# Optimization experiments

Hardware: AMD Instinct MI355X
Metric: run time of the kernel (lower is better)

## Reference

```python
import jax, jax.numpy as jnp
import numpy as np

B, T, D = 2, 1024, 1024
H, DK, DV = 16, 64, 128   # head_dim=64, head_v_dim=128 (expand_v=2)
F_HID, CONV = 2816, 4
EPS = 1e-6


def rmsnorm(x, w, eps=EPS):
    return x * jax.lax.rsqrt(jnp.mean(x * x, -1, keepdims=True) + eps) * w


def l2norm(x, eps=1e-6):
    return x * jax.lax.rsqrt(jnp.sum(x * x, -1, keepdims=True) + eps)


def short_conv(x, w):
    # causal depthwise conv1d (kernel CONV, no bias) + silu; x: [B,T,C], w: [C,K]
    K = w.shape[1]
    xp = jnp.pad(x, ((0, 0), (K - 1, 0), (0, 0)))
    y = jax.lax.conv_general_dilated(
        xp, w.T[:, None, :], (1,), 'VALID',
        dimension_numbers=('NWC', 'WIO', 'NWC'), feature_group_count=w.shape[0])
    return jax.nn.silu(y)


def gated_delta_rule(q, k, v, g, beta):
    # q,k: [B,T,H,DK], v: [B,T,H,DV], g,beta: [B,T,H]
    scale = q.shape[-1] ** -0.5
    q = l2norm(q) * scale
    k = l2norm(k)

    def step(S, inp):
        qt, kt, vt, gt, bt = inp          # S: [B,H,DK,DV]
        S = S * jnp.exp(gt)[..., None, None]
        err = jnp.einsum('bhk,bhkv->bhv', kt, S)
        vt = (vt - err) * bt[..., None]
        S = S + kt[..., :, None] * vt[..., None, :]
        ot = jnp.einsum('bhk,bhkv->bhv', qt, S)
        return S, ot

    S0 = jnp.zeros((q.shape[0], H, DK, DV), q.dtype)
    inputs = tuple(jnp.moveaxis(a, 1, 0) for a in (q, k, v, g, beta))
    _, o = jax.lax.scan(step, S0, inputs)
    return jnp.moveaxis(o, 0, 1)  # [B,T,H,DV]


def setup_inputs():
    key = jax.random.key(0)
    ks = jax.random.split(key, 20)
    w = lambda k, shape, s=0.02: jax.random.normal(k, shape, jnp.float32) * s
    return {
        'x': jax.random.normal(ks[0], (B, T, D), jnp.float32),
        'norm1_w': jnp.ones((D,), jnp.float32),
        'norm2_w': jnp.ones((D,), jnp.float32),
        'Wq': w(ks[1], (D, H * DK)),
        'Wk': w(ks[2], (D, H * DK)),
        'Wv': w(ks[3], (D, H * DV)),
        'conv_q': w(ks[4], (H * DK, CONV), 0.3),
        'conv_k': w(ks[5], (H * DK, CONV), 0.3),
        'conv_v': w(ks[6], (H * DV, CONV), 0.3),
        'Wa': w(ks[7], (D, H)),
        'Wb': w(ks[8], (D, H)),
        'dt_bias': jnp.log(jnp.expm1(jax.random.uniform(ks[9], (H,), minval=0.001, maxval=0.1))),
        'A_log': jnp.log(jax.random.uniform(ks[10], (H,), minval=1.0, maxval=16.0)),
        'Wg': w(ks[11], (D, H * DV)),
        'o_norm_w': jnp.ones((DV,), jnp.float32),
        'Wo': w(ks[12], (H * DV, D)),
        'W1': w(ks[13], (D, F_HID)),
        'W3': w(ks[14], (D, F_HID)),
        'W2': w(ks[15], (F_HID, D)),
    }


def reference(x, norm1_w, norm2_w, Wq, Wk, Wv, conv_q, conv_k, conv_v,
              Wa, Wb, dt_bias, A_log, Wg, o_norm_w, Wo, W1, W3, W2):
    # --- pre-norm + GatedDeltaNet ---
    h = rmsnorm(x, norm1_w)
    q = short_conv(h @ Wq, conv_q).reshape(B, T, H, DK)
    k = short_conv(h @ Wk, conv_k).reshape(B, T, H, DK)
    v = short_conv(h @ Wv, conv_v).reshape(B, T, H, DV)
    beta = jax.nn.sigmoid(h @ Wb)                                  # [B,T,H]
    g = -jnp.exp(A_log) * jax.nn.softplus(h @ Wa + dt_bias)       # [B,T,H] decay log
    o = gated_delta_rule(q, k, v, g, beta)                         # [B,T,H,DV]
    gate = (h @ Wg).reshape(B, T, H, DV)
    o = rmsnorm(o, o_norm_w, 1e-5) * jax.nn.silu(gate)             # gated RMSNorm
    x = x + o.reshape(B, T, H * DV) @ Wo                           # residual 1
    # --- pre-norm + SwiGLU FFN ---
    h2 = rmsnorm(x, norm2_w)
    ffn = (jax.nn.silu(h2 @ W1) * (h2 @ W3)) @ W2
    return x + ffn
```

## Files before the change

### kernel.cpp

```cpp
#include <hip/hip_runtime.h>
#include <hip/hip_bf16.h>
#include <math.h>

#define B_  2
#define T_  1024
#define D_  1024
#define H_  16
#define DK_ 64
#define DV_ 128
#define FH_ 2816
#define M_  (B_ * T_)
#define C_  64
#define NCH (T_ / C_)

typedef __attribute__((ext_vector_type(8))) short bf16x8;
typedef __attribute__((ext_vector_type(4))) float f32x4;

__global__ __launch_bounds__(256) void rmsnorm_k(
    const float* __restrict__ x, const float* __restrict__ w,
    float* __restrict__ outf, __hip_bfloat16* __restrict__ outb,
    int D, float eps) {
  const int row = blockIdx.x;
  const float* xr = x + (size_t)row * D;
  float ss = 0.f;
  for (int i = threadIdx.x; i < D; i += blockDim.x) { float v = xr[i]; ss += v * v; }
  for (int off = 32; off > 0; off >>= 1) ss += __shfl_xor(ss, off, 64);
  __shared__ float wsum[4];
  __shared__ float s_scale;
  const int lane = threadIdx.x & 63, wid = threadIdx.x >> 6;
  if (lane == 0) wsum[wid] = ss;
  __syncthreads();
  if (threadIdx.x == 0) {
    float tot = 0.f;
    const int nw = blockDim.x >> 6;
    for (int i = 0; i < nw; ++i) tot += wsum[i];
    s_scale = rsqrtf(tot / (float)D + eps);
  }
  __syncthreads();
  const float sc = s_scale;
  for (int i = threadIdx.x; i < D; i += blockDim.x) {
    const float v = xr[i] * sc * w[i];
    if (outf) outf[(size_t)row * D + i] = v;
    if (outb) outb[(size_t)row * D + i] = __float2bfloat16(v);
  }
}

__global__ __launch_bounds__(256) void transpose_bf16_k(
    const float* __restrict__ W, __hip_bfloat16* __restrict__ Wt, int K, int N) {
  __shared__ float t[32][33];
  const int k0 = blockIdx.y * 32, n0 = blockIdx.x * 32;
  const int c = threadIdx.x & 31, r = threadIdx.x >> 5;
#pragma unroll
  for (int i = 0; i < 4; ++i)
    t[r + 8 * i][c] = W[(size_t)(k0 + r + 8 * i) * N + n0 + c];
  __syncthreads();
#pragma unroll
  for (int i = 0; i < 4; ++i)
    Wt[(size_t)(n0 + r + 8 * i) * K + k0 + c] = __float2bfloat16(t[c][r + 8 * i]);
}

__device__ __forceinline__ void gload_lds16(const void* g, void* l) {
  __builtin_amdgcn_global_load_lds(
      (const __attribute__((address_space(1))) void*)g,
      (__attribute__((address_space(3))) void*)l, 16, 0, 0);
}

template<int BM, int BN>
__global__ __launch_bounds__(256) void mfma_gemm_k(
    const __hip_bfloat16* __restrict__ A, const __hip_bfloat16* __restrict__ Bt,
    const float* __restrict__ res, void* __restrict__ Cout,
    int M, int N, int K, int mode) {
  __shared__ __hip_bfloat16 As[2][BM * 64];
  __shared__ __hip_bfloat16 Bs[2][BN * 64];
  constexpr int MF = BM / 32;
  constexpr int NF = BN / 32;
  const int tid = threadIdx.x;
  const int lane = tid & 63;
  const int wv = tid >> 6;
  const int wm = (wv >> 1) * (BM / 2), wn = (wv & 1) * (BN / 2);
  const int bm = blockIdx.y * BM, bn = blockIdx.x * BN;
  const int l15 = lane & 15, lq8 = (lane >> 4) * 8;
  const int ar = tid >> 2;
  const int ac = (tid & 3) * 8;
  const size_t Abase = (size_t)(bm + ar) * K + ac;
  const size_t Bbase = (size_t)(bn + ar) * K + ac;
  f32x4 acc[MF][NF];
#pragma unroll
  for (int i = 0; i < MF; ++i)
#pragma unroll
    for (int j = 0; j < NF; ++j) acc[i][j] = (f32x4){0.f, 0.f, 0.f, 0.f};

  auto stage = [&](int buf, int k0) {
#pragma unroll
    for (int s = 0; s < 2; ++s) {
      const int kk = k0 + 32 * s;
      char* dA = (char*)&As[buf][s * BM * 32] + tid * 16;
      gload_lds16(A + Abase + kk, dA);
      if constexpr (BM == 128)
        gload_lds16(A + Abase + (size_t)64 * K + kk, dA + 4096);
      char* dB = (char*)&Bs[buf][s * BN * 32] + tid * 16;
      gload_lds16(Bt + Bbase + kk, dB);
      if constexpr (BN == 128)
        gload_lds16(Bt + Bbase + (size_t)64 * K + kk, dB + 4096);
    }
  };

  stage(0, 0);
  __syncthreads();
  int cur = 0;
#pragma unroll 2
  for (int k0 = 0; k0 < K; k0 += 64) {
    if (k0 + 64 < K) stage(cur ^ 1, k0 + 64);
#pragma unroll
    for (int s = 0; s < 2; ++s) {
      bf16x8 af[MF], bfr[NF];
#pragma unroll
      for (int i = 0; i < MF; ++i)
        af[i] = *(const bf16x8*)(&As[cur][s * BM * 32] + (wm + i * 16 + l15) * 32 + lq8);
#pragma unroll
      for (int j = 0; j < NF; ++j)
        bfr[j] = *(const bf16x8*)(&Bs[cur][s * BN * 32] + (wn + j * 16 + l15) * 32 + lq8);
#pragma unroll
      for (int i = 0; i < MF; ++i)
#pragma unroll
        for (int j = 0; j < NF; ++j)
          acc[i][j] = __builtin_amdgcn_mfma_f32_16x16x32_bf16(af[i], bfr[j], acc[i][j], 0, 0, 0);
    }
    __syncthreads();
    cur ^= 1;
  }
  const int r0 = (lane >> 4) * 4;
#pragma unroll
  for (int i = 0; i < MF; ++i) {
#pragma unroll
    for (int j = 0; j < NF; ++j) {
      const int row = bm + wm + i * 16 + r0;
      const int col = bn + wn + j * 16 + l15;
#pragma unroll
      for (int r = 0; r < 4; ++r) {
        const size_t idx = (size_t)(row + r) * N + col;
        const float a = acc[i][j][r];
        if (mode == 0) ((float*)Cout)[idx] = a;
        else if (mode == 1) ((float*)Cout)[idx] = a + res[idx];
        else {
          const float s = res[idx];
          ((__hip_bfloat16*)Cout)[idx] =
              __float2bfloat16(s * (1.f / (1.f + __expf(-s))) * a);
        }
      }
    }
  }
}

__global__ __launch_bounds__(256) void skinny_k(
    const float* __restrict__ h, const float* __restrict__ Wa,
    const float* __restrict__ Wb, float* __restrict__ pa,
    float* __restrict__ pb, int K) {
  __shared__ float hl[D_];
  __shared__ float red[8][32];
  const int row = blockIdx.x;
  const int tid = threadIdx.x;
  {
    const float4* src = (const float4*)(h + (size_t)row * K);
    ((float4*)hl)[tid] = src[tid];
  }
  __syncthreads();
  const int col = tid & 31, sub = tid >> 5;
  const float* W = (col < 16) ? Wa : Wb;
  const int cc = col & 15;
  float s = 0.f;
  const int kk0 = sub * 128;
  for (int k = kk0; k < kk0 + 128; ++k) s += hl[k] * W[k * H_ + cc];
  red[sub][col] = s;
  __syncthreads();
  if (tid < 32) {
    float t = 0.f;
#pragma unroll
    for (int i = 0; i < 8; ++i) t += red[i][tid];
    if (tid < 16) pa[(size_t)row * H_ + tid] = t;
    else          pb[(size_t)row * H_ + tid - 16] = t;
  }
}

__global__ __launch_bounds__(256) void conv_silu_k(
    const float* __restrict__ src, const float* __restrict__ w,
    float* __restrict__ dst, int C, int sstr, int soff) {
  const int bt = blockIdx.x;
  const int b = bt / T_, t = bt % T_;
  const float* s = src + (size_t)b * T_ * sstr + soff;
  for (int c = threadIdx.x; c < C; c += blockDim.x) {
    const float w0 = w[c * 4 + 0], w1 = w[c * 4 + 1],
                w2 = w[c * 4 + 2], w3 = w[c * 4 + 3];
    float acc = s[(size_t)t * sstr + c] * w3;
    if (t >= 1) acc += s[(size_t)(t - 1) * sstr + c] * w2;
    if (t >= 2) acc += s[(size_t)(t - 2) * sstr + c] * w1;
    if (t >= 3) acc += s[(size_t)(t - 3) * sstr + c] * w0;
    dst[(size_t)bt * C + c] = acc * (1.f / (1.f + __expf(-acc)));
  }
}

__global__ void beta_g_k(const float* __restrict__ pa, const float* __restrict__ pb,
                         const float* __restrict__ dtb, const float* __restrict__ Alog,
                         float* __restrict__ g, float* __restrict__ beta, int n) {
  const int i = blockIdx.x * blockDim.x + threadIdx.x;
  if (i >= n) return;
  const int h = i & (H_ - 1);
  const float xx = pa[i] + dtb[h];
  const float sp = (xx > 20.f) ? xx : log1pf(expf(xx));
  g[i] = -expf(Alog[h]) * sp;
  beta[i] = 1.f / (1.f + expf(-pb[i]));
}

__global__ __launch_bounds__(64) void l2norm_k(float* __restrict__ q, float scale) {
  const size_t row = blockIdx.x;
  const int lane = threadIdx.x;
  const float v = q[row * 64 + lane];
  float ss = v * v;
  for (int off = 32; off > 0; off >>= 1) ss += __shfl_xor(ss, off, 64);
  q[row * 64 + lane] = v * rsqrtf(ss + 1e-6f) * scale;
}

__global__ __launch_bounds__(256) void chunk_prep_k(
    const float* __restrict__ q, float* __restrict__ k, float* __restrict__ v,
    const float* __restrict__ g, const float* __restrict__ beta,
    float* __restrict__ qkd, float* __restrict__ kdt, float* __restrict__ gam,
    float* __restrict__ wt) {
  const int task = blockIdx.x;
  const int bh = task >> 4, n = task & (NCH - 1);
  const int b = bh >> 4, h = bh & 15;
  const int t0 = n * C_;
  const int tid = threadIdx.x;
  __shared__ float lk[C_][68];
  __shared__ float Gs[C_][68];
  __shared__ float Xs[C_][100];
  __shared__ float Td[4][16][17];
  __shared__ float lb[C_], lgam[C_], lbeta[C_], lbg[C_];
  {
    const int r = tid >> 2, cq = (tid & 3) * 16;
    const float* src = k + (((size_t)b * T_ + t0 + r) * H_ + h) * DK_ + cq;
#pragma unroll
    for (int i = 0; i < 4; ++i)
      *(float4*)&lk[r][cq + 4 * i] = ((const float4*)src)[i];
  }
  if (tid < 64) {
    const size_t gi = ((size_t)b * T_ + t0 + tid) * H_ + h;
    float xx = g[gi];
    const float bb = beta[gi];
    lbeta[tid] = bb;
#pragma unroll
    for (int off = 1; off < 64; off <<= 1) {
      float y = __shfl_up(xx, off, 64);
      if (tid >= off) xx += y;
    }
    lb[tid] = xx;
    const float gm = __expf(xx);
    lgam[tid] = gm;
    lbg[tid] = bb * gm;
  }
  __syncthreads();
  const int r4g = (tid >> 4) * 4;
  const int sl = tid & 15;
  {
    const float* qg = q + (((size_t)b * T_ + t0) * H_ + h) * DK_;
    float accA[4][4] = {};
    float accQ[4][4] = {};
    for (int d = 0; d < 64; d += 4) {
      float4 kt[4], ks[4], qt[4];
#pragma unroll
      for (int i = 0; i < 4; ++i) kt[i] = *(const float4*)&lk[r4g + i][d];
#pragma unroll
      for (int j = 0; j < 4; ++j) ks[j] = *(const float4*)&lk[sl + 16 * j][d];
#pragma unroll
      for (int i = 0; i < 4; ++i) qt[i] = *(const float4*)(qg + (size_t)(r4g + i) * (H_ * DK_) + d);
#pragma unroll
      for (int i = 0; i < 4; ++i)
#pragma unroll
        for (int j = 0; j < 4; ++j) {
          accA[i][j] += kt[i].x * ks[j].x + kt[i].y * ks[j].y + kt[i].z * ks[j].z + kt[i].w * ks[j].w;
          accQ[i][j] += qt[i].x * ks[j].x + qt[i].y * ks[j].y + qt[i].z * ks[j].z + qt[i].w * ks[j].w;
        }
    }
    float* qo = qkd + (size_t)task * 4096;
#pragma unroll
    for (int i = 0; i < 4; ++i)
#pragma unroll
      for (int j = 0; j < 4; ++j) {
        const int t = r4g + i, s = sl + 16 * j;
        const float dec = (s <= t) ? __expf(lb[t] - lb[s]) : 0.f;
        Gs[t][s] = (t > s) ? lbeta[t] * accA[i][j] * dec : 0.f;
        qo[t * 64 + s] = accQ[i][j] * dec;
      }
  }
  {
    const int s = tid >> 2, dq = (tid & 3) * 16;
    const float e = __expf(lb[63] - lb[s]);
    float* dst = kdt + (size_t)task * 4096 + s * 64 + dq;
#pragma unroll
    for (int m = 0; m < 4; ++m) {
      float4 kv = *(const float4*)&lk[s][dq + 4 * m];
      kv.x *= e; kv.y *= e; kv.z *= e; kv.w *= e;
      *(float4*)(dst + 4 * m) = kv;
    }
  }
  if (tid < 64) gam[(size_t)task * 64 + tid] = lgam[tid];
  __syncthreads();
  if (tid < 64) {
    const int blk = tid >> 4, cI = tid & 15;
    float Xc[16];
#pragma unroll
    for (int t = 0; t < 16; ++t) Xc[t] = (t == cI) ? 1.f : 0.f;
#pragma unroll
    for (int t = 1; t < 16; ++t) {
      float acc = 0.f;
#pragma unroll
      for (int s = 0; s < t; ++s)
        acc += Gs[blk * 16 + t][blk * 16 + s] * Xc[s];
      Xc[t] -= acc;
    }
#pragma unroll
    for (int t = 0; t < 16; ++t) Td[blk][t][cI] = Xc[t];
  } else {
    for (int idx = tid - 64; idx < 64 * 96; idx += 192) {
      const int t = idx / 96, c = idx % 96;
      Xs[t][c] = lbeta[t] * v[(((size_t)b * T_ + t0 + t) * H_ + h) * DV_ + c];
    }
  }
  __syncthreads();
  const int rt = tid & 15;
  const int cg = tid >> 4;
#pragma unroll 1
  for (int half = 0; half < 2; ++half) {
#pragma unroll
    for (int bi = 0; bi < 4; ++bi) {
      if (bi > 0) {
        float acc[6] = {0.f, 0.f, 0.f, 0.f, 0.f, 0.f};
        for (int kk = 0; kk < 16 * bi; ++kk) {
          const float gvv = Gs[16 * bi + rt][kk];
#pragma unroll
          for (int c = 0; c < 6; ++c) acc[c] += gvv * Xs[kk][cg * 6 + c];
        }
#pragma unroll
        for (int c = 0; c < 6; ++c) Xs[16 * bi + rt][cg * 6 + c] -= acc[c];
      }
      float y[6] = {0.f, 0.f, 0.f, 0.f, 0.f, 0.f};
#pragma unroll
      for (int s = 0; s < 16; ++s) {
        const float tv = Td[bi][rt][s];
#pragma unroll
        for (int c = 0; c < 6; ++c) y[c] += tv * Xs[16 * bi + s][cg * 6 + c];
      }
#pragma unroll
      for (int c = 0; c < 6; ++c) Xs[16 * bi + rt][cg * 6 + c] = y[c];
    }
    __syncthreads();
    if (half == 0) {
      for (int idx = tid; idx < 64 * 96; idx += 256) {
        const int t = idx / 96, c = idx % 96;
        v[(((size_t)b * T_ + t0 + t) * H_ + h) * DV_ + c] = Xs[t][c];
      }
      __syncthreads();
      for (int idx = tid; idx < 64 * 96; idx += 256) {
        const int t = idx / 96, c = idx % 96;
        if (c < 32)
          Xs[t][c] = lbeta[t] * v[(((size_t)b * T_ + t0 + t) * H_ + h) * DV_ + 96 + c];
        else
          Xs[t][c] = lbg[t] * lk[t][c - 32];
      }
      __syncthreads();
    } else {
      for (int idx = tid; idx < 64 * 32; idx += 256) {
        const int t = idx >> 5, cc = idx & 31;
        v[(((size_t)b * T_ + t0 + t) * H_ + h) * DV_ + 96 + cc] = Xs[t][cc];
      }
      {
        const int dk = tid & 63, tg = tid >> 6;
        float buf[16];
#pragma unroll
        for (int j = 0; j < 16; ++j) buf[j] = Xs[16 * tg + j][32 + dk];
        float* dst = wt + (size_t)task * 4096 + dk * 64 + 16 * tg;
#pragma unroll
        for (int m = 0; m < 4; ++m)
          *(float4*)(dst + 4 * m) =
              make_float4(buf[4 * m], buf[4 * m + 1], buf[4 * m + 2], buf[4 * m + 3]);
      }
    }
  }
}

__global__ __launch_bounds__(256) void chunk_rec_k(
    const float* __restrict__ WT, float* __restrict__ u,
    const float* __restrict__ kdtT, const float* __restrict__ gam,
    float* __restrict__ Sst) {
  const int bh = blockIdx.x & 31, cg = blockIdx.x >> 5;
  const int b = bh >> 4, h = bh & 15;
  const int c0 = cg * 16;
  const int tid = threadIdx.x;
  const int w = tid >> 6;
  const int lane = tid & 63;
  const int L15 = lane & 15;
  const int t4 = L15 * 4;
  const int c = w * 4 + (lane >> 4);
  const int iot = tid >> 2;
  const int ioq = (tid & 3) * 4;

  __shared__ float Wt[2][64 * 64];
  __shared__ float Kt[2][64 * 64];
  __shared__ float SsT[16][68];
  __shared__ float UbT[16][68];
  __shared__ float Ub0[64][17];

  float Sr[4];
#pragma unroll
  for (int i = 0; i < 4; ++i) Sr[i] = 0.f;
#pragma unroll
  for (int i = 0; i < 4; ++i) SsT[c][t4 + i] = 0.f;

  {
    const float* sW = WT + (size_t)(bh * NCH) * 4096 + w * 1024 + lane * 4;
    const float* sK = kdtT + (size_t)(bh * NCH) * 4096 + w * 1024 + lane * 4;
    char* lW = (char*)&Wt[0][w * 1024] + lane * 16;
    char* lK = (char*)&Kt[0][w * 1024] + lane * 16;
#pragma unroll
    for (int i = 0; i < 4; ++i) {
      gload_lds16(sW + i * 256, lW + i * 1024);
      gload_lds16(sK + i * 256, lK + i * 1024);
    }
  }
  __syncthreads();

#pragma unroll 1
  for (int n = 0; n < NCH; ++n) {
    const int cur = n & 1, nx = cur ^ 1;
    const int task = bh * NCH + n;
    const int t0 = n * C_;
    const int n1 = (n + 1 < NCH) ? n + 1 : NCH - 1;
    const int task1 = bh * NCH + n1;
    const float gC = gam[(size_t)task * 64 + 63];

    const float4 uv = *(const float4*)(
        u + (((size_t)b * T_ + t0 + iot) * H_ + h) * DV_ + c0 + ioq);
    {
      const float* sW = WT + (size_t)task1 * 4096 + w * 1024 + lane * 4;
      const float* sK = kdtT + (size_t)task1 * 4096 + w * 1024 + lane * 4;
      char* lW = (char*)&Wt[nx][w * 1024] + lane * 16;
      char* lK = (char*)&Kt[nx][w * 1024] + lane * 16;
#pragma unroll
      for (int i = 0; i < 4; ++i) {
        gload_lds16(sW + i * 256, lW + i * 1024);
        gload_lds16(sK + i * 256, lK + i * 1024);
      }
    }
    __builtin_amdgcn_sched_barrier(0);
    {
      float4 sv;
      sv.x = SsT[ioq + 0][iot]; sv.y = SsT[ioq + 1][iot];
      sv.z = SsT[ioq + 2][iot]; sv.w = SsT[ioq + 3][iot];
      *(float4*)(Sst + (size_t)task * 8192 + iot * 128 + c0 + ioq) = sv;
    }
    float4 srow[16];
#pragma unroll
    for (int g = 0; g < 16; ++g) srow[g] = *(const float4*)&SsT[c][4 * g];
    float acc[4] = {0.f, 0.f, 0.f, 0.f};
#pragma unroll
    for (int g = 0; g < 16; ++g) {
      const float sj[4] = {srow[g].x, srow[g].y, srow[g].z, srow[g].w};
#pragma unroll
      for (int j = 0; j < 4; ++j) {
        const float4 wv = *(const float4*)&Wt[cur][(4 * g + j) * 64 + t4];
        acc[0] += wv.x * sj[j]; acc[1] += wv.y * sj[j];
        acc[2] += wv.z * sj[j]; acc[3] += wv.w * sj[j];
      }
    }
    Ub0[iot][ioq + 0] = uv.x; Ub0[iot][ioq + 1] = uv.y;
    Ub0[iot][ioq + 2] = uv.z; Ub0[iot][ioq + 3] = uv.w;
    __syncthreads();

#pragma unroll
    for (int i = 0; i < 4; ++i)
      UbT[c][t4 + i] = Ub0[t4 + i][c] - acc[i];
    float4 urow[16];
#pragma unroll
    for (int g = 0; g < 16; ++g) urow[g] = *(const float4*)&UbT[c][4 * g];
    float ac2[4] = {0.f, 0.f, 0.f, 0.f};
#pragma unroll
    for (int g = 0; g < 16; ++g) {
      const float uj[4] = {urow[g].x, urow[g].y, urow[g].z, urow[g].w};
#pragma unroll
      for (int j = 0; j < 4; ++j) {
        const float4 kv = *(const float4*)&Kt[cur][(4 * g + j) * 64 + t4];
        ac2[0] += kv.x * uj[j]; ac2[1] += kv.y * uj[j];
        ac2[2] += kv.z * uj[j]; ac2[3] += kv.w * uj[j];
      }
    }
#pragma unroll
    for (int i = 0; i < 4; ++i) {
      Sr[i] = gC * Sr[i] + ac2[i];
      SsT[c][t4 + i] = Sr[i];
    }
    __syncthreads();

    {
      float4 ov;
      ov.x = UbT[ioq + 0][iot]; ov.y = UbT[ioq + 1][iot];
      ov.z = UbT[ioq + 2][iot]; ov.w = UbT[ioq + 3][iot];
      *(float4*)(u + (((size_t)b * T_ + t0 + iot) * H_ + h) * DV_ + c0 + ioq) = ov;
    }
  }
}

__global__ __launch_bounds__(128) void chunk_o_k(
    const float* __restrict__ q, const float* __restrict__ qkd,
    const float* __restrict__ ub, const float* __restrict__ Sst,
    const float* __restrict__ gam, const float* __restrict__ gate,
    const float* __restrict__ onw, __hip_bfloat16* __restrict__ go) {
  const int task = blockIdx.x;
  const int bh = task >> 4, n = task & 15;
  const int b = bh >> 4, h = bh & 15;
  const int t0 = n * C_;
  const int tid = threadIdx.x;
  const int rowg = tid >> 4, colg = tid & 15;
  const int r8 = rowg * 8, c4 = colg * 4;
  __shared__ float At[64][68];
  __shared__ float Bs[64][132];
  __shared__ float lgam[64];
  if (tid < 64) lgam[tid] = gam[(size_t)task * 64 + tid];
  __syncthreads();
  const int t2 = tid >> 1, dh = (tid & 1) * 32;
  {
    const float* src = q + (((size_t)b * T_ + t0 + t2) * H_ + h) * DK_ + dh;
    const float sc = lgam[t2];
#pragma unroll
    for (int i = 0; i < 8; ++i) {
      const float4 v = ((const float4*)src)[i];
      At[dh + 4 * i + 0][t2] = v.x * sc; At[dh + 4 * i + 1][t2] = v.y * sc;
      At[dh + 4 * i + 2][t2] = v.z * sc; At[dh + 4 * i + 3][t2] = v.w * sc;
    }
  }
  {
    const float* src = Sst + (size_t)task * 8192 + t2 * 128 + (tid & 1) * 64;
    float* dst = &Bs[t2][(tid & 1) * 64];
#pragma unroll
    for (int i = 0; i < 16; ++i) ((float4*)dst)[i] = ((const float4*)src)[i];
  }
  __syncthreads();
  float acc[8][8];
#pragma unroll
  for (int i = 0; i < 8; ++i)
#pragma unroll
    for (int c = 0; c < 8; ++c) acc[i][c] = 0.f;
#pragma unroll 1
  for (int ph = 0; ph < 2; ++ph) {
    for (int kb = 0; kb < 64; kb += 4) {
#pragma unroll
      for (int j = 0; j < 4; ++j) {
        const float4 alo = *(const float4*)&At[kb + j][r8];
        const float4 ahi = *(const float4*)&At[kb + j][r8 + 4];
        const float4 blo = *(const float4*)&Bs[kb + j][c4];
        const float4 bhi = *(const float4*)&Bs[kb + j][c4 + 64];
        const float av[8] = {alo.x, alo.y, alo.z, alo.w, ahi.x, ahi.y, ahi.z, ahi.w};
        const float bv[8] = {blo.x, blo.y, blo.z, blo.w, bhi.x, bhi.y, bhi.z, bhi.w};
#pragma unroll
        for (int i = 0; i < 8; ++i)
#pragma unroll
          for (int c = 0; c < 8; ++c) acc[i][c] += av[i] * bv[c];
      }
    }
    if (ph == 0) {
      __syncthreads();
      {
        const float* src = qkd + (size_t)task * 4096 + t2 * 64 + dh;
#pragma unroll
        for (int i = 0; i < 8; ++i) {
          const float4 v = ((const float4*)src)[i];
          At[dh + 4 * i + 0][t2] = v.x; At[dh + 4 * i + 1][t2] = v.y;
          At[dh + 4 * i + 2][t2] = v.z; At[dh + 4 * i + 3][t2] = v.w;
        }
      }
      {
        const float* src = ub + (((size_t)b * T_ + t0 + t2) * H_ + h) * DV_ + (tid & 1) * 64;
        float* dst = &Bs[t2][(tid & 1) * 64];
#pragma unroll
        for (int i = 0; i < 16; ++i) ((float4*)dst)[i] = ((const float4*)src)[i];
      }
      __syncthreads();
    }
  }
#pragma unroll
  for (int i = 0; i < 8; ++i) {
    float pr = 0.f;
#pragma unroll
    for (int c = 0; c < 8; ++c) pr += acc[i][c] * acc[i][c];
    pr += __shfl_xor(pr, 1, 64);
    pr += __shfl_xor(pr, 2, 64);
    pr += __shfl_xor(pr, 4, 64);
    pr += __shfl_xor(pr, 8, 64);
    const float rms = rsqrtf(pr / (float)DV_ + 1e-5f);
    const size_t rb = (((size_t)b * T_ + t0 + r8 + i) * H_ + h) * DV_;
    const float4 glo = *(const float4*)(gate + rb + c4);
    const float4 ghi = *(const float4*)(gate + rb + c4 + 64);
    const float gv[8] = {glo.x, glo.y, glo.z, glo.w, ghi.x, ghi.y, ghi.z, ghi.w};
    unsigned short outv[8];
#pragma unroll
    for (int c = 0; c < 8; ++c) {
      const int col = (c < 4) ? c4 + c : c4 + 60 + c;
      const float gg = gv[c];
      const float val = acc[i][c] * rms * onw[col] * gg * (1.f / (1.f + __expf(-gg)));
      const __hip_bfloat16 bfv = __float2bfloat16(val);
      outv[c] = *(const unsigned short*)&bfv;
    }
    *(ushort4*)((unsigned short*)go + rb + c4) =
        make_ushort4(outv[0], outv[1], outv[2], outv[3]);
    *(ushort4*)((unsigned short*)go + rb + c4 + 64) =
        make_ushort4(outv[4], outv[5], outv[6], outv[7]);
  }
}

extern "C" void kernel_launch(void* const* d_in, const int* in_sizes, int n_in,
                              void* d_out, int out_size, void* d_ws, size_t ws_size,
                              hipStream_t stream) {
  const float* x    = (const float*)d_in[0];
  const float* n1w  = (const float*)d_in[1];
  const float* n2w  = (const float*)d_in[2];
  const float* Wq   = (const float*)d_in[3];
  const float* Wk   = (const float*)d_in[4];
  const float* Wv   = (const float*)d_in[5];
  const float* cq   = (const float*)d_in[6];
  const float* ck   = (const float*)d_in[7];
  const float* cv   = (const float*)d_in[8];
  const float* Wa   = (const float*)d_in[9];
  const float* Wb   = (const float*)d_in[10];
  const float* dtb  = (const float*)d_in[11];
  const float* Alog = (const float*)d_in[12];
  const float* Wg   = (const float*)d_in[13];
  const float* onw  = (const float*)d_in[14];
  const float* Wo   = (const float*)d_in[15];
  const float* W1   = (const float*)d_in[16];
  const float* W3   = (const float*)d_in[17];
  const float* W2   = (const float*)d_in[18];
  float* out = (float*)d_out;
  float* ws  = (float*)d_ws;

  const size_t SZ_MD = (size_t)M_ * D_;
  const size_t SZ_MV = (size_t)M_ * H_ * DV_;
  float* h    = ws;
  float* pq   = ws + SZ_MD;
  float* pk   = ws + 2 * SZ_MD;
  float* pv   = ws + 3 * SZ_MD;
  float* gate = ws + 3 * SZ_MD + SZ_MV;
  float* qb   = ws + 3 * SZ_MD + 2 * SZ_MV;
  float* kb   = ws + 4 * SZ_MD + 2 * SZ_MV;
  float* vb   = ws + 5 * SZ_MD + 2 * SZ_MV;
  float* Sst  = pv;
  float* y1   = pq;
  float* a1   = pv;
  float* wtb  = h;
  float* proj = pq;
  float* smalls = ws + 5 * SZ_MD + 3 * SZ_MV;
  float* pa  = smalls;
  float* pb  = pa + (size_t)M_ * H_;
  float* gv  = pb + (size_t)M_ * H_;
  float* bv  = gv + (size_t)M_ * H_;
  float* gam = bv + (size_t)M_ * H_;
  __hip_bfloat16* h_bf  = (__hip_bfloat16*)vb;
  __hip_bfloat16* wb1   = (__hip_bfloat16*)kb;
  __hip_bfloat16* wb2   = (__hip_bfloat16*)vb;
  __hip_bfloat16* go_bf = (__hip_bfloat16*)h;
  __hip_bfloat16* h2_bf = (__hip_bfloat16*)h;
  __hip_bfloat16* a1b   = (__hip_bfloat16*)qb;

  const dim3 blk256(256);
  const dim3 g_tr1024_1024(1024 / 32, 1024 / 32);
  const dim3 g_tr1024_2048(2048 / 32, 1024 / 32);
  const dim3 g_tr2048_1024(1024 / 32, 2048 / 32);
  const dim3 g_tr1024_2816(2816 / 32, 1024 / 32);
  const dim3 g_tr2816_1024(1024 / 32, 2816 / 32);

  rmsnorm_k<<<dim3(M_), blk256, 0, stream>>>(x, n1w, h, h_bf, D_, 1e-6f);
  transpose_bf16_k<<<g_tr1024_1024, blk256, 0, stream>>>(Wq, wb1, D_, 1024);
  transpose_bf16_k<<<g_tr1024_1024, blk256, 0, stream>>>(Wk, wb1 + (size_t)1024 * 1024, D_, 1024);
  transpose_bf16_k<<<g_tr1024_2048, blk256, 0, stream>>>(Wv, wb1 + (size_t)2048 * 1024, D_, 2048);
  mfma_gemm_k<128, 128><<<dim3(4096 / 128, M_ / 128), blk256, 0, stream>>>(h_bf, wb1, nullptr, proj, M_, 4096, D_, 0);
  transpose_bf16_k<<<g_tr1024_2048, blk256, 0, stream>>>(Wg, wb1, D_, 2048);
  mfma_gemm_k<128, 64><<<dim3(2048 / 64, M_ / 128), blk256, 0, stream>>>(h_bf, wb1, nullptr, gate, M_, 2048, D_, 0);
  skinny_k<<<dim3(M_), blk256, 0, stream>>>(h, Wa, Wb, pa, pb, D_);
  conv_silu_k<<<dim3(M_), blk256, 0, stream>>>(proj, cq, qb, H_ * DK_, 4096, 0);
  conv_silu_k<<<dim3(M_), blk256, 0, stream>>>(proj, ck, kb, H_ * DK_, 4096, 1024);
  conv_silu_k<<<dim3(M_), blk256, 0, stream>>>(proj, cv, vb, H_ * DV_, 4096, 2048);
  beta_g_k<<<dim3((M_ * H_ + 255) / 256), blk256, 0, stream>>>(pa, pb, dtb, Alog, gv, bv, M_ * H_);
  l2norm_k<<<dim3(M_ * H_), dim3(64), 0, stream>>>(qb, 0.125f);
  l2norm_k<<<dim3(M_ * H_), dim3(64), 0, stream>>>(kb, 1.0f);
  chunk_prep_k<<<dim3(32 * NCH), blk256, 0, stream>>>(qb, kb, vb, gv, bv, pq, pk, gam, wtb);
  chunk_rec_k<<<dim3(256), blk256, 0, stream>>>(wtb, vb, pk, gam, Sst);
  chunk_o_k<<<dim3(32 * NCH), dim3(128), 0, stream>>>(qb, pq, vb, Sst, gam, gate, onw, go_bf);
  transpose_bf16_k<<<g_tr2048_1024, blk256, 0, stream>>>(Wo, wb2, H_ * DV_, 1024);
  mfma_gemm_k<64, 64><<<dim3(1024 / 64, M_ / 64), blk256, 0, stream>>>(go_bf, wb2, x, y1, M_, 1024, H_ * DV_, 1);
  rmsnorm_k<<<dim3(M_), blk256, 0, stream>>>(y1, n2w, nullptr, h2_bf, D_, 1e-6f);
  transpose_bf16_k<<<g_tr1024_2816, blk256, 0, stream>>>(W1, wb2, D_, FH_);
  mfma_gemm_k<128, 64><<<dim3(FH_ / 64, M_ / 128), blk256, 0, stream>>>(h2_bf, wb2, nullptr, a1, M_, FH_, D_, 0);
  transpose_bf16_k<<<g_tr1024_2816, blk256, 0, stream>>>(W3, wb2, D_, FH_);
  mfma_gemm_k<128, 64><<<dim3(FH_ / 64, M_ / 128), blk256, 0, stream>>>(h2_bf, wb2, a1, a1b, M_, FH_, D_, 2);
  transpose_bf16_k<<<g_tr2816_1024, blk256, 0, stream>>>(W2, wb2, FH_, 1024);
  mfma_gemm_k<64, 64><<<dim3(1024 / 64, M_ / 64), blk256, 0, stream>>>(a1b, wb2, y1, out, M_, 1024, FH_, 1);
}
```

Baseline: 558.2 us.

## Fuse small elementwise kernels and batch weight transposes to cut launches

Merges the first RMSNorm with the skinny Wa/Wb projection and the beta/g activation into one kernel. It also fuses the three conv+SiLU launches and the two l2norm launches, and batches the weight transposes into multi-matrix launches. The goal is to remove kernel launch overhead and a few intermediate round trips through global memory. In exchange, buffer aliasing gets tighter: W1 and W3 are transposed ahead of time into a larger region of the vb/wb2 workspace, and Wg into qb, which relies on those regions being large enough and not still in use.

```diff
diff --git a/kernel.cpp b/kernel.cpp
--- a/kernel.cpp
+++ b/kernel.cpp
@@ -45,10 +45,78 @@
   }
 }
 
-__global__ __launch_bounds__(256) void transpose_bf16_k(
-    const float* __restrict__ W, __hip_bfloat16* __restrict__ Wt, int K, int N) {
+__global__ __launch_bounds__(256) void rms_skinny_k(
+    const float* __restrict__ x, const float* __restrict__ n1w,
+    const float* __restrict__ Wa, const float* __restrict__ Wb,
+    const float* __restrict__ dtb, const float* __restrict__ Alog,
+    float* __restrict__ hout, __hip_bfloat16* __restrict__ houtb,
+    float* __restrict__ gv, float* __restrict__ bv) {
+  __shared__ float hl[D_];
+  __shared__ float red[8][32];
+  __shared__ float wsum[4];
+  __shared__ float s_scale;
+  const int row = blockIdx.x;
+  const int tid = threadIdx.x;
+  const float* xr = x + (size_t)row * D_;
+  float ss = 0.f;
+  for (int i = tid; i < D_; i += 256) { float v = xr[i]; ss += v * v; }
+  for (int off = 32; off > 0; off >>= 1) ss += __shfl_xor(ss, off, 64);
+  const int lane = tid & 63, wid = tid >> 6;
+  if (lane == 0) wsum[wid] = ss;
+  __syncthreads();
+  if (tid == 0) {
+    float tot = wsum[0] + wsum[1] + wsum[2] + wsum[3];
+    s_scale = rsqrtf(tot / (float)D_ + 1e-6f);
+  }
+  __syncthreads();
+  const float sc = s_scale;
+  for (int i = tid; i < D_; i += 256) {
+    const float v = xr[i] * sc * n1w[i];
+    hout[(size_t)row * D_ + i] = v;
+    houtb[(size_t)row * D_ + i] = __float2bfloat16(v);
+    hl[i] = v;
+  }
+  __syncthreads();
+  const int col = tid & 31, sub = tid >> 5;
+  const float* W = (col < 16) ? Wa : Wb;
+  const int cc = col & 15;
+  float s = 0.f;
+  const int kk0 = sub * 128;
+  for (int k = kk0; k < kk0 + 128; ++k) s += hl[k] * W[k * H_ + cc];
+  red[sub][col] = s;
+  __syncthreads();
+  if (tid < 32) {
+    float t = 0.f;
+#pragma unroll
+    for (int i = 0; i < 8; ++i) t += red[i][tid];
+    if (tid < 16) {
+      const float xx = t + dtb[tid];
+      const float sp = (xx > 20.f) ? xx : log1pf(expf(xx));
+      gv[(size_t)row * H_ + tid] = -expf(Alog[tid]) * sp;
+    } else {
+      bv[(size_t)row * H_ + tid - 16] = 1.f / (1.f + expf(-t));
+    }
+  }
+}
+
+__global__ __launch_bounds__(256) void transpose_multi_k(
+    const float* __restrict__ s0, const float* __restrict__ s1,
+    const float* __restrict__ s2, const float* __restrict__ s3,
+    __hip_bfloat16* __restrict__ d0, __hip_bfloat16* __restrict__ d1,
+    __hip_bfloat16* __restrict__ d2, __hip_bfloat16* __restrict__ d3,
+    int K0, int N0, int K1, int N1, int K2, int N2, int K3, int N3,
+    int e1, int e2, int e3) {
   __shared__ float t[32][33];
-  const int k0 = blockIdx.y * 32, n0 = blockIdx.x * 32;
+  int tb = blockIdx.x;
+  const float* W;
+  __hip_bfloat16* Wt;
+  int K, N;
+  if (tb < e1)      { W = s0; Wt = d0; K = K0; N = N0; }
+  else if (tb < e2) { W = s1; Wt = d1; K = K1; N = N1; tb -= e1; }
+  else if (tb < e3) { W = s2; Wt = d2; K = K2; N = N2; tb -= e2; }
+  else              { W = s3; Wt = d3; K = K3; N = N3; tb -= e3; }
+  const int tpr = N >> 5;
+  const int k0 = (tb / tpr) * 32, n0 = (tb % tpr) * 32;
   const int c = threadIdx.x & 31, r = threadIdx.x >> 5;
 #pragma unroll
   for (int i = 0; i < 4; ++i)
@@ -152,72 +220,45 @@
   }
 }
 
-__global__ __launch_bounds__(256) void skinny_k(
-    const float* __restrict__ h, const float* __restrict__ Wa,
-    const float* __restrict__ Wb, float* __restrict__ pa,
-    float* __restrict__ pb, int K) {
-  __shared__ float hl[D_];
-  __shared__ float red[8][32];
-  const int row = blockIdx.x;
-  const int tid = threadIdx.x;
-  {
-    const float4* src = (const float4*)(h + (size_t)row * K);
-    ((float4*)hl)[tid] = src[tid];
-  }
-  __syncthreads();
-  const int col = tid & 31, sub = tid >> 5;
-  const float* W = (col < 16) ? Wa : Wb;
-  const int cc = col & 15;
-  float s = 0.f;
-  const int kk0 = sub * 128;
-  for (int k = kk0; k < kk0 + 128; ++k) s += hl[k] * W[k * H_ + cc];
-  red[sub][col] = s;
-  __syncthreads();
-  if (tid < 32) {
-    float t = 0.f;
-#pragma unroll
-    for (int i = 0; i < 8; ++i) t += red[i][tid];
-    if (tid < 16) pa[(size_t)row * H_ + tid] = t;
-    else          pb[(size_t)row * H_ + tid - 16] = t;
-  }
-}
-
-__global__ __launch_bounds__(256) void conv_silu_k(
-    const float* __restrict__ src, const float* __restrict__ w,
-    float* __restrict__ dst, int C, int sstr, int soff) {
+__global__ __launch_bounds__(256) void conv_fused_k(
+    const float* __restrict__ proj, const float* __restrict__ cq,
+    const float* __restrict__ ck, const float* __restrict__ cv,
+    float* __restrict__ qb, float* __restrict__ kb, float* __restrict__ vb) {
   const int bt = blockIdx.x;
   const int b = bt / T_, t = bt % T_;
-  const float* s = src + (size_t)b * T_ * sstr + soff;
-  for (int c = threadIdx.x; c < C; c += blockDim.x) {
-    const float w0 = w[c * 4 + 0], w1 = w[c * 4 + 1],
-                w2 = w[c * 4 + 2], w3 = w[c * 4 + 3];
-    float acc = s[(size_t)t * sstr + c] * w3;
-    if (t >= 1) acc += s[(size_t)(t - 1) * sstr + c] * w2;
-    if (t >= 2) acc += s[(size_t)(t - 2) * sstr + c] * w1;
-    if (t >= 3) acc += s[(size_t)(t - 3) * sstr + c] * w0;
-    dst[(size_t)bt * C + c] = acc * (1.f / (1.f + __expf(-acc)));
-  }
-}
-
-__global__ void beta_g_k(const float* __restrict__ pa, const float* __restrict__ pb,
-                         const float* __restrict__ dtb, const float* __restrict__ Alog,
-                         float* __restrict__ g, float* __restrict__ beta, int n) {
-  const int i = blockIdx.x * blockDim.x + threadIdx.x;
-  if (i >= n) return;
-  const int h = i & (H_ - 1);
-  const float xx = pa[i] + dtb[h];
-  const float sp = (xx > 20.f) ? xx : log1pf(expf(xx));
-  g[i] = -expf(Alog[h]) * sp;
-  beta[i] = 1.f / (1.f + expf(-pb[i]));
-}
-
-__global__ __launch_bounds__(64) void l2norm_k(float* __restrict__ q, float scale) {
+  const float* s = proj + (size_t)b * T_ * 4096;
+  const int tid = threadIdx.x;
+#pragma unroll 1
+  for (int seg = 0; seg < 3; ++seg) {
+    const int C = (seg == 2) ? 2048 : 1024;
+    const int off = (seg == 0) ? 0 : (seg == 1 ? 1024 : 2048);
+    const float* w = (seg == 0) ? cq : (seg == 1 ? ck : cv);
+    float* dst = (seg == 0) ? qb : (seg == 1 ? kb : vb);
+    for (int c = tid; c < C; c += 256) {
+      const float w0 = w[c * 4 + 0], w1 = w[c * 4 + 1],
+                  w2 = w[c * 4 + 2], w3 = w[c * 4 + 3];
+      float acc = s[(size_t)t * 4096 + off + c] * w3;
+      if (t >= 1) acc += s[(size_t)(t - 1) * 4096 + off + c] * w2;
+      if (t >= 2) acc += s[(size_t)(t - 2) * 4096 + off + c] * w1;
+      if (t >= 3) acc += s[(size_t)(t - 3) * 4096 + off + c] * w0;
+      dst[(size_t)bt * C + c] = acc * (1.f / (1.f + __expf(-acc)));
+    }
+  }
+}
+
+__global__ __launch_bounds__(64) void l2norm2_k(float* __restrict__ q,
+                                                float* __restrict__ k) {
   const size_t row = blockIdx.x;
+  const size_t nq = (size_t)M_ * H_;
+  float* p;
+  float scale;
+  if (row < nq) { p = q + row * 64; scale = 0.125f; }
+  else          { p = k + (row - nq) * 64; scale = 1.0f; }
   const int lane = threadIdx.x;
-  const float v = q[row * 64 + lane];
+  const float v = p[lane];
   float ss = v * v;
   for (int off = 32; off > 0; off >>= 1) ss += __shfl_xor(ss, off, 64);
-  q[row * 64 + lane] = v * rsqrtf(ss + 1e-6f) * scale;
+  p[lane] = v * rsqrtf(ss + 1e-6f) * scale;
 }
 
 __global__ __launch_bounds__(256) void chunk_prep_k(
@@ -656,49 +697,46 @@
   float* wtb  = h;
   float* proj = pq;
   float* smalls = ws + 5 * SZ_MD + 3 * SZ_MV;
-  float* pa  = smalls;
-  float* pb  = pa + (size_t)M_ * H_;
-  float* gv  = pb + (size_t)M_ * H_;
+  float* gv  = smalls;
   float* bv  = gv + (size_t)M_ * H_;
   float* gam = bv + (size_t)M_ * H_;
   __hip_bfloat16* h_bf  = (__hip_bfloat16*)vb;
   __hip_bfloat16* wb1   = (__hip_bfloat16*)kb;
+  __hip_bfloat16* wgt   = (__hip_bfloat16*)qb;
   __hip_bfloat16* wb2   = (__hip_bfloat16*)vb;
   __hip_bfloat16* go_bf = (__hip_bfloat16*)h;
   __hip_bfloat16* h2_bf = (__hip_bfloat16*)h;
   __hip_bfloat16* a1b   = (__hip_bfloat16*)qb;
 
   const dim3 blk256(256);
-  const dim3 g_tr1024_1024(1024 / 32, 1024 / 32);
-  const dim3 g_tr1024_2048(2048 / 32, 1024 / 32);
-  const dim3 g_tr2048_1024(1024 / 32, 2048 / 32);
-  const dim3 g_tr1024_2816(2816 / 32, 1024 / 32);
-  const dim3 g_tr2816_1024(1024 / 32, 2816 / 32);
-
-  rmsnorm_k<<<dim3(M_), blk256, 0, stream>>>(x, n1w, h, h_bf, D_, 1e-6f);
-  transpose_bf16_k<<<g_tr1024_1024, blk256, 0, stream>>>(Wq, wb1, D_, 1024);
-  transpose_bf16_k<<<g_tr1024_1024, blk256, 0, stream>>>(Wk, wb1 + (size_t)1024 * 1024, D_, 1024);
-  transpose_bf16_k<<<g_tr1024_2048, blk256, 0, stream>>>(Wv, wb1 + (size_t)2048 * 1024, D_, 2048);
+
+  rms_skinny_k<<<dim3(M_), blk256, 0, stream>>>(x, n1w, Wa, Wb, dtb, Alog, h, h_bf, gv, bv);
+  transpose_multi_k<<<dim3(6144), blk256, 0, stream>>>(
+      Wq, Wk, Wv, Wg,
+      wb1, wb1 + (size_t)1024 * 1024, wb1 + (size_t)2048 * 1024, wgt,
+      1024, 1024, 1024, 1024, 1024, 2048, 1024, 2048,
+      1024, 2048, 4096);
   mfma_gemm_k<128, 128><<<dim3(4096 / 128, M_ / 128), blk256, 0, stream>>>(h_bf, wb1, nullptr, proj, M_, 4096, D_, 0);
-  transpose_bf16_k<<<g_tr1024_2048, blk256, 0, stream>>>(Wg, wb1, D_, 2048);
-  mfma_gemm_k<128, 64><<<dim3(2048 / 64, M_ / 128), blk256, 0, stream>>>(h_bf, wb1, nullptr, gate, M_, 2048, D_, 0);
-  skinny_k<<<dim3(M_), blk256, 0, stream>>>(h, Wa, Wb, pa, pb, D_);
-  conv_silu_k<<<dim3(M_), blk256, 0, stream>>>(proj, cq, qb, H_ * DK_, 4096, 0);
-  conv_silu_k<<<dim3(M_), blk256, 0, stream>>>(proj, ck, kb, H_ * DK_, 4096, 1024);
-  conv_silu_k<<<dim3(M_), blk256, 0, stream>>>(proj, cv, vb, H_ * DV_, 4096, 2048);
-  beta_g_k<<<dim3((M_ * H_ + 255) / 256), blk256, 0, stream>>>(pa, pb, dtb, Alog, gv, bv, M_ * H_);
-  l2norm_k<<<dim3(M_ * H_), dim3(64), 0, stream>>>(qb, 0.125f);
-  l2norm_k<<<dim3(M_ * H_), dim3(64), 0, stream>>>(kb, 1.0f);
+  mfma_gemm_k<128, 64><<<dim3(2048 / 64, M_ / 128), blk256, 0, stream>>>(h_bf, wgt, nullptr, gate, M_, 2048, D_, 0);
+  conv_fused_k<<<dim3(M_), blk256, 0, stream>>>(proj, cq, ck, cv, qb, kb, vb);
+  l2norm2_k<<<dim3(2 * M_ * H_), dim3(64), 0, stream>>>(qb, kb);
   chunk_prep_k<<<dim3(32 * NCH), blk256, 0, stream>>>(qb, kb, vb, gv, bv, pq, pk, gam, wtb);
   chunk_rec_k<<<dim3(256), blk256, 0, stream>>>(wtb, vb, pk, gam, Sst);
   chunk_o_k<<<dim3(32 * NCH), dim3(128), 0, stream>>>(qb, pq, vb, Sst, gam, gate, onw, go_bf);
-  transpose_bf16_k<<<g_tr2048_1024, blk256, 0, stream>>>(Wo, wb2, H_ * DV_, 1024);
+  transpose_multi_k<<<dim3(7680), blk256, 0, stream>>>(
+      Wo, W1, W3, Wo,
+      wb2, wb2 + (size_t)2048 * 1024, wb2 + (size_t)4864 * 1024, wb2,
+      2048, 1024, 1024, 2816, 1024, 2816, 32, 32,
+      2048, 4864, 7680);
   mfma_gemm_k<64, 64><<<dim3(1024 / 64, M_ / 64), blk256, 0, stream>>>(go_bf, wb2, x, y1, M_, 1024, H_ * DV_, 1);
   rmsnorm_k<<<dim3(M_), blk256, 0, stream>>>(y1, n2w, nullptr, h2_bf, D_, 1e-6f);
-  transpose_bf16_k<<<g_tr1024_2816, blk256, 0, stream>>>(W1, wb2, D_, FH_);
-  mfma_gemm_k<128, 64><<<dim3(FH_ / 64, M_ / 128), blk256, 0, stream>>>(h2_bf, wb2, nullptr, a1, M_, FH_, D_, 0);
-  transpose_bf16_k<<<g_tr1024_2816, blk256, 0, stream>>>(W3, wb2, D_, FH_);
-  mfma_gemm_k<128, 64><<<dim3(FH_ / 64, M_ / 128), blk256, 0, stream>>>(h2_bf, wb2, a1, a1b, M_, FH_, D_, 2);
-  transpose_bf16_k<<<g_tr2816_1024, blk256, 0, stream>>>(W2, wb2, FH_, 1024);
+  mfma_gemm_k<128, 64><<<dim3(FH_ / 64, M_ / 128), blk256, 0, stream>>>(
+      h2_bf, wb2 + (size_t)2048 * 1024, nullptr, a1, M_, FH_, D_, 0);
+  mfma_gemm_k<128, 64><<<dim3(FH_ / 64, M_ / 128), blk256, 0, stream>>>(
+      h2_bf, wb2 + (size_t)4864 * 1024, a1, a1b, M_, FH_, D_, 2);
+  transpose_multi_k<<<dim3(2816), blk256, 0, stream>>>(
+      W2, W2, W2, W2, wb2, wb2, wb2, wb2,
+      2816, 1024, 2816, 1024, 2816, 1024, 2816, 1024,
+      2816, 2816, 2816);
   mfma_gemm_k<64, 64><<<dim3(1024 / 64, M_ / 64), blk256, 0, stream>>>(a1b, wb2, y1, out, M_, 1024, FH_, 1);
 }
```

New measurement: 515.2 us. -7.7%, faster.
